# Optimization experiments

Hardware: AMD Instinct MI355X
Metric: run time of the kernel (lower is better)

The kernel has to match this reference:

```python
import jax, jax.numpy as jnp
import numpy as np

B, L, D, DIN, S, R, K = 2, 1024, 1024, 2048, 16, 64, 4


def setup_inputs() -> dict:
    key = jax.random.key(0)
    ks = jax.random.split(key, 8)
    f = lambda k, sh, sc: jax.random.normal(k, sh, jnp.float32) * sc
    return {
        "x": f(ks[0], (B, L, D), 1.0),
        "norm_w": jnp.ones((D,), jnp.float32),
        "W_in": f(ks[1], (D, 2 * DIN), D ** -0.5),
        "conv_w": f(ks[2], (DIN, 1, K), 0.5),
        "conv_b": jnp.zeros((DIN,), jnp.float32),
        "W_x": f(ks[3], (DIN, R + 2 * S), DIN ** -0.5),
        "W_dt": f(ks[4], (R, DIN), R ** -0.5),
        "b_dt": f(ks[5], (DIN,), 0.1),
        "A_log": jnp.log(jnp.broadcast_to(jnp.arange(1, S + 1, dtype=jnp.float32), (DIN, S))),
        "D_skip": jnp.ones((DIN,), jnp.float32),
        "W_out": f(ks[6], (DIN, D), DIN ** -0.5),
    }


def reference(x, norm_w, W_in, conv_w, conv_b, W_x, W_dt, b_dt, A_log, D_skip, W_out):
    eps = 1e-5
    # RMSNorm
    xn = x * jax.lax.rsqrt(jnp.mean(x * x, axis=-1, keepdims=True) + eps) * norm_w
    # input projection -> (x_branch, gate)
    xz = xn @ W_in                       # [B,L,2*DIN]
    xi, z = jnp.split(xz, 2, axis=-1)
    # causal depthwise conv1d along L
    xt = jnp.transpose(xi, (0, 2, 1))    # [B,DIN,L]
    xc = jax.lax.conv_general_dilated(xt, conv_w, (1,), [(K - 1, 0)],
                                      feature_group_count=DIN)
    xc = jnp.transpose(xc, (0, 2, 1)) + conv_b
    xc = jax.nn.silu(xc)                 # [B,L,DIN]
    # input-dependent SSM parameters
    xd = xc @ W_x                        # [B,L,R+2S]
    dt, Bm, Cm = jnp.split(xd, [R, R + S], axis=-1)
    dt = jax.nn.softplus(dt @ W_dt + b_dt)           # [B,L,DIN]
    A = -jnp.exp(A_log)                              # [DIN,S]
    dA = jnp.exp(dt[..., None] * A)                  # [B,L,DIN,S]
    dBu = (dt * xc)[..., None] * Bm[:, :, None, :]   # [B,L,DIN,S]
    # selective scan: h_t = dA_t * h_{t-1} + dBu_t (parallel associative scan)
    def comb(c1, c2):
        a1, b1 = c1
        a2, b2 = c2
        return a1 * a2, a2 * b1 + b2
    _, h = jax.lax.associative_scan(comb, (dA, dBu), axis=1)
    y = jnp.einsum('blds,bls->bld', h, Cm) + D_skip * xc
    y = y * jax.nn.silu(z)
    return x + y @ W_out
```

## Files before the change

kernel.cpp:

```cpp
#include <hip/hip_runtime.h>

#define B_    2
#define L_    1024
#define D_    1024
#define DIN_  2048
#define S_    16
#define R_    64
#define NTOK  (B_ * L_)
#define NCH   32
#define LC    (L_ / NCH)

typedef unsigned short u16;
typedef short bf16x8 __attribute__((ext_vector_type(8)));
typedef float f32x4  __attribute__((ext_vector_type(4)));

__device__ __forceinline__ u16 f2bf(float f) {
    union { float f; unsigned u; } v; v.f = f;
    return (u16)((v.u + 0x7FFFu + ((v.u >> 16) & 1u)) >> 16);
}
__device__ __forceinline__ float bf2f(u16 b) {
    union { unsigned u; float f; } v; v.u = (unsigned)b << 16;
    return v.f;
}

__global__ __launch_bounds__(256) void rmsnorm_kernel(
    const float* __restrict__ x, const float* __restrict__ w, u16* __restrict__ xn) {
    int row = blockIdx.x;
    const float4 v = ((const float4*)(x + (size_t)row * D_))[threadIdx.x];
    float ss = v.x * v.x + v.y * v.y + v.z * v.z + v.w * v.w;
#pragma unroll
    for (int o = 32; o > 0; o >>= 1) ss += __shfl_down(ss, o);
    __shared__ float red[4];
    if ((threadIdx.x & 63) == 0) red[threadIdx.x >> 6] = ss;
    __syncthreads();
    float tot = red[0] + red[1] + red[2] + red[3];
    float sc = rsqrtf(tot * (1.f / (float)D_) + 1e-5f);
    const float4 wv = ((const float4*)w)[threadIdx.x];
    ushort4 o;
    o.x = f2bf(v.x * sc * wv.x);
    o.y = f2bf(v.y * sc * wv.y);
    o.z = f2bf(v.z * sc * wv.z);
    o.w = f2bf(v.w * sc * wv.w);
    ((ushort4*)(xn + (size_t)row * D_))[threadIdx.x] = o;
}

__device__ __forceinline__ void transp_tile(
    const float* __restrict__ src, u16* __restrict__ dst,
    int R, int Csrc, int cx, int cy, int tx, int ty) {
    __shared__ float tile[32][33];
    int c0 = cx * 32, r0 = cy * 32;
#pragma unroll
    for (int i = 0; i < 32; i += 8)
        tile[ty + i][tx] = (c0 + tx < Csrc)
            ? src[(size_t)(r0 + ty + i) * Csrc + c0 + tx] : 0.f;
    __syncthreads();
#pragma unroll
    for (int i = 0; i < 32; i += 8)
        dst[(size_t)(c0 + ty + i) * R + r0 + tx] = f2bf(tile[tx][ty + i]);
}

__global__ __launch_bounds__(256) void transpose_all_kernel(
    const float* __restrict__ W_in,  u16* __restrict__ WinT,
    const float* __restrict__ W_out, u16* __restrict__ WoutT,
    const float* __restrict__ W_x,   u16* __restrict__ WxT,
    const float* __restrict__ W_dt,  u16* __restrict__ WdtT) {
    int bid = blockIdx.x;
    int tx = threadIdx.x & 31, ty = threadIdx.x >> 5;
    if (bid < 4096) {
        transp_tile(W_in, WinT, D_, 2 * DIN_, bid % 128, bid / 128, tx, ty);
    } else if (bid < 6144) {
        int b = bid - 4096;
        transp_tile(W_out, WoutT, DIN_, D_, b % 32, b / 32, tx, ty);
    } else if (bid < 6400) {
        int b = bid - 6144;
        transp_tile(W_x, WxT, DIN_, 96, b % 4, b / 4, tx, ty);
    } else {
        int b = bid - 6400;
        transp_tile(W_dt, WdtT, R_, DIN_, b % 64, b / 64, tx, ty);
    }
}

#define BK 32
template<int BM, int BN, int CX>
__global__ __launch_bounds__(256) void gemm_bf16(
    const u16* __restrict__ A, int lda,
    const u16* __restrict__ Bt, int ldb,
    float* __restrict__ C, u16* __restrict__ Cbf, int ldc,
    const float* __restrict__ aux,
    int M, int N, int K, int mode) {
    constexpr int WGM = (BM >= 128) ? 2 : 1;
    constexpr int WGN = 4 / WGM;
    constexpr int FM = BM / (16 * WGM);
    constexpr int FN = BN / (16 * WGN);
    constexpr int ABYTES = BM * BK * 2;
    constexpr int BBYTES = BN * BK * 2;
    __shared__ __align__(16) u16 As[2][BM * BK];
    __shared__ __align__(16) u16 Bs[2][BN * BK];
    const int t = threadIdx.x;
    const int w = t >> 6;
    const int l = t & 63;
    const int lr = l & 15;
    const int kg = l >> 4;
    const int wm = (w / WGN) * (BM / WGM);
    const int wn = (w % WGN) * (BN / WGN);

    const int GX = gridDim.x, GY = gridDim.y;
    int h = blockIdx.x + GX * (blockIdx.y + GY * blockIdx.z);
    int xcd = h & 7, pos = h >> 3;
    int ncx = GX / CX;
    int chunk = (GX * GY * gridDim.z) >> 3;
    int rpc = chunk / CX;
    int bx = (xcd % ncx) * CX + pos % CX;
    int r  = (xcd / ncx) * rpc + pos / CX;
    int by = r % GY;
    int bz = r / GY;

    const int row0 = by * BM;
    const int col0 = bx * BN;
    const int kbase = bz * K;

    auto stage = [&](int buf, int k0) {
#pragma unroll
        for (int i = 0; i < ABYTES; i += 4096) {
            int off = i + t * 16;
            int grow = off >> 6;
            int sw = ((off >> 4) & 3) ^ ((grow >> 1) & 3);
            const u16* ga = A + (size_t)(row0 + grow) * lda + k0 + sw * 8;
            __builtin_amdgcn_global_load_lds(
                (const __attribute__((address_space(1))) unsigned int*)(const void*)ga,
                (__attribute__((address_space(3))) unsigned int*)(void*)&As[buf][off >> 1],
                16, 0, 0);
        }
#pragma unroll
        for (int i = 0; i < BBYTES; i += 4096) {
            int off = i + t * 16;
            int grow = off >> 6;
            int sw = ((off >> 4) & 3) ^ ((grow >> 1) & 3);
            const u16* gb = Bt + (size_t)(col0 + grow) * ldb + k0 + sw * 8;
            __builtin_amdgcn_global_load_lds(
                (const __attribute__((address_space(1))) unsigned int*)(const void*)gb,
                (__attribute__((address_space(3))) unsigned int*)(void*)&Bs[buf][off >> 1],
                16, 0, 0);
        }
    };

    f32x4 acc[FM][FN];
#pragma unroll
    for (int i = 0; i < FM; ++i)
#pragma unroll
        for (int j = 0; j < FN; ++j) acc[i][j] = (f32x4){0.f, 0.f, 0.f, 0.f};

    const int nt = K / BK;
    stage(0, kbase);
    asm volatile("s_waitcnt vmcnt(0)" ::: "memory");
    __builtin_amdgcn_s_barrier();
    asm volatile("" ::: "memory");

    int cur = 0;
    for (int tt = 0; tt < nt; ++tt) {
        if (tt + 1 < nt) stage(cur ^ 1, kbase + (tt + 1) * BK);
        bf16x8 af[FM], bfr[FN];
#pragma unroll
        for (int mt = 0; mt < FM; ++mt) {
            int ar = wm + mt * 16 + lr;
            af[mt] = *(const bf16x8*)&As[cur][ar * 32 + (kg ^ ((ar >> 1) & 3)) * 8];
        }
#pragma unroll
        for (int nt2 = 0; nt2 < FN; ++nt2) {
            int br = wn + nt2 * 16 + lr;
            bfr[nt2] = *(const bf16x8*)&Bs[cur][br * 32 + (kg ^ ((br >> 1) & 3)) * 8];
        }
        __builtin_amdgcn_s_setprio(1);
#pragma unroll
        for (int mt = 0; mt < FM; ++mt)
#pragma unroll
            for (int nt2 = 0; nt2 < FN; ++nt2)
                acc[mt][nt2] = __builtin_amdgcn_mfma_f32_16x16x32_bf16(
                    af[mt], bfr[nt2], acc[mt][nt2], 0, 0, 0);
        __builtin_amdgcn_s_setprio(0);
        if (tt + 1 < nt) {
            asm volatile("s_waitcnt vmcnt(0)" ::: "memory");
            __builtin_amdgcn_s_barrier();
            asm volatile("" ::: "memory");
        }
        cur ^= 1;
    }

    size_t pbase = (mode == 3) ? (size_t)bz * M * N : 0;
#pragma unroll
    for (int mt = 0; mt < FM; ++mt) {
#pragma unroll
        for (int nt2 = 0; nt2 < FN; ++nt2) {
#pragma unroll
            for (int r2 = 0; r2 < 4; ++r2) {
                int row = row0 + wm + mt * 16 + kg * 4 + r2;
                int col = col0 + wn + nt2 * 16 + lr;
                float v = acc[mt][nt2][r2];
                if (mode == 1) { v += aux[col]; v = (v > 20.f) ? v : log1pf(__expf(v)); }
                else if (mode == 2) { v += aux[(size_t)row * ldc + col]; }
                if (C)   C[pbase + (size_t)row * ldc + col] = v;
                if (Cbf) Cbf[(size_t)row * ldc + col] = f2bf(v);
            }
        }
    }
}

__global__ __launch_bounds__(256) void reduce_wx_kernel(
    const float* __restrict__ part, float* __restrict__ xd, u16* __restrict__ xdb) {
    int i = blockIdx.x * 256 + threadIdx.x;
    float4 s = ((const float4*)part)[i];
#pragma unroll
    for (int k = 1; k < 16; ++k) {
        float4 v = ((const float4*)(part + (size_t)k * NTOK * 128))[i];
        s.x += v.x; s.y += v.y; s.z += v.z; s.w += v.w;
    }
    ((float4*)xd)[i] = s;
    ushort4 o; o.x = f2bf(s.x); o.y = f2bf(s.y); o.z = f2bf(s.z); o.w = f2bf(s.w);
    ((ushort4*)xdb)[i] = o;
}

__global__ __launch_bounds__(256) void reduce_out_kernel(
    const float* __restrict__ part, const float* __restrict__ x, float* __restrict__ out) {
    int i = blockIdx.x * 256 + threadIdx.x;
    float4 s = ((const float4*)part)[i];
#pragma unroll
    for (int k = 1; k < 4; ++k) {
        float4 v = ((const float4*)(part + (size_t)k * NTOK * D_))[i];
        s.x += v.x; s.y += v.y; s.z += v.z; s.w += v.w;
    }
    float4 xv = ((const float4*)x)[i];
    s.x += xv.x; s.y += xv.y; s.z += xv.z; s.w += xv.w;
    ((float4*)out)[i] = s;
}

__global__ __launch_bounds__(256) void conv_silu_kernel(
    const float* __restrict__ xz, const float* __restrict__ cw,
    const float* __restrict__ cb, u16* __restrict__ xcb) {
    size_t idx = (size_t)blockIdx.x * 256 + threadIdx.x;
    int c = (int)(idx & (DIN_ - 1));
    int g = (int)(idx >> 11);
    int bl0 = g * 4;
    int l0 = bl0 & (L_ - 1);
    const float4 w = ((const float4*)cw)[c];
    float bias = cb[c];
    float v[7];
#pragma unroll
    for (int k = 0; k < 7; ++k) {
        int off = k - 3;
        v[k] = (l0 + off >= 0) ? xz[(size_t)(bl0 + off) * 4096 + c] : 0.f;
    }
#pragma unroll
    for (int j = 0; j < 4; ++j) {
        float acc = bias + v[j] * w.x + v[j + 1] * w.y + v[j + 2] * w.z + v[j + 3] * w.w;
        float s = acc / (1.f + __expf(-acc));
        xcb[(size_t)(bl0 + j) * DIN_ + c] = f2bf(s);
    }
}

__global__ __launch_bounds__(256) void scan_chunk_kernel(
    const float* __restrict__ dt, const u16* __restrict__ xcb,
    const float* __restrict__ xd, const float* __restrict__ A_log,
    float* __restrict__ Pout, float* __restrict__ Hout) {
    int din = blockIdx.x * 256 + threadIdx.x;
    int c = blockIdx.y, b = blockIdx.z;
    float a[S_], h[S_];
#pragma unroll
    for (int q = 0; q < 4; ++q) {
        float4 av = ((const float4*)(A_log + (size_t)din * S_))[q];
        a[q * 4 + 0] = -__expf(av.x); a[q * 4 + 1] = -__expf(av.y);
        a[q * 4 + 2] = -__expf(av.z); a[q * 4 + 3] = -__expf(av.w);
    }
#pragma unroll
    for (int s = 0; s < S_; ++s) h[s] = 0.f;
    float sdt = 0.f;
    size_t rbase = (size_t)b * L_ + (size_t)c * LC;
#pragma unroll 2
    for (int i = 0; i < LC; ++i) {
        size_t row = rbase + i;
        float dtv = dt[row * DIN_ + din];
        float xcv = bf2f(xcb[row * DIN_ + din]);
        float du = dtv * xcv;
        sdt += dtv;
        const float4* bp = (const float4*)(xd + row * 128 + 64);
        float4 B0 = bp[0], B1 = bp[1], B2 = bp[2], B3 = bp[3];
        float Bv[S_] = {B0.x, B0.y, B0.z, B0.w, B1.x, B1.y, B1.z, B1.w,
                        B2.x, B2.y, B2.z, B2.w, B3.x, B3.y, B3.z, B3.w};
#pragma unroll
        for (int s = 0; s < S_; ++s) {
            float dA = __expf(dtv * a[s]);
            h[s] = h[s] * dA + du * Bv[s];
        }
    }
    size_t obase = ((size_t)(b * NCH + c) * DIN_ + din) * S_;
#pragma unroll
    for (int q = 0; q < 4; ++q) {
        float4 pv, hv;
        pv.x = __expf(a[q * 4 + 0] * sdt); pv.y = __expf(a[q * 4 + 1] * sdt);
        pv.z = __expf(a[q * 4 + 2] * sdt); pv.w = __expf(a[q * 4 + 3] * sdt);
        hv.x = h[q * 4 + 0]; hv.y = h[q * 4 + 1]; hv.z = h[q * 4 + 2]; hv.w = h[q * 4 + 3];
        ((float4*)(Pout + obase))[q] = pv;
        ((float4*)(Hout + obase))[q] = hv;
    }
}

__global__ __launch_bounds__(256) void scan_combine_kernel(
    const float* __restrict__ P, const float* __restrict__ H,
    float* __restrict__ h0) {
    int tid = blockIdx.x * 256 + threadIdx.x;
    int ds = tid & (DIN_ * S_ - 1);
    int b = tid >> 15;
    float h = 0.f;
#pragma unroll
    for (int c = 0; c < NCH; ++c) {
        size_t idx = ((size_t)(b * NCH + c) * DIN_ * S_) + ds;
        h0[idx] = h;
        h = H[idx] + P[idx] * h;
    }
}

__global__ __launch_bounds__(256) void scan_final_kernel(
    const float* __restrict__ dt, const u16* __restrict__ xcb,
    const float* __restrict__ xd, const float* __restrict__ A_log,
    const float* __restrict__ h0, const float* __restrict__ Dskip,
    const float* __restrict__ xz, u16* __restrict__ yg) {
    int din = blockIdx.x * 256 + threadIdx.x;
    int c = blockIdx.y, b = blockIdx.z;
    float a[S_], h[S_];
#pragma unroll
    for (int q = 0; q < 4; ++q) {
        float4 av = ((const float4*)(A_log + (size_t)din * S_))[q];
        a[q * 4 + 0] = -__expf(av.x); a[q * 4 + 1] = -__expf(av.y);
        a[q * 4 + 2] = -__expf(av.z); a[q * 4 + 3] = -__expf(av.w);
    }
    size_t ibase = ((size_t)(b * NCH + c) * DIN_ + din) * S_;
#pragma unroll
    for (int q = 0; q < 4; ++q) {
        float4 hv = ((const float4*)(h0 + ibase))[q];
        h[q * 4 + 0] = hv.x; h[q * 4 + 1] = hv.y; h[q * 4 + 2] = hv.z; h[q * 4 + 3] = hv.w;
    }
    float dsk = Dskip[din];
    size_t rbase = (size_t)b * L_ + (size_t)c * LC;
#pragma unroll 2
    for (int i = 0; i < LC; ++i) {
        size_t row = rbase + i;
        float dtv = dt[row * DIN_ + din];
        float xcv = bf2f(xcb[row * DIN_ + din]);
        float du = dtv * xcv;
        const float4* bp = (const float4*)(xd + row * 128 + 64);
        float4 B0 = bp[0], B1 = bp[1], B2 = bp[2], B3 = bp[3];
        const float4* cp = (const float4*)(xd + row * 128 + 80);
        float4 C0 = cp[0], C1 = cp[1], C2 = cp[2], C3 = cp[3];
        float Bv[S_] = {B0.x, B0.y, B0.z, B0.w, B1.x, B1.y, B1.z, B1.w,
                        B2.x, B2.y, B2.z, B2.w, B3.x, B3.y, B3.z, B3.w};
        float Cv[S_] = {C0.x, C0.y, C0.z, C0.w, C1.x, C1.y, C1.z, C1.w,
                        C2.x, C2.y, C2.z, C2.w, C3.x, C3.y, C3.z, C3.w};
        float py = 0.f;
#pragma unroll
        for (int s = 0; s < S_; ++s) {
            float dA = __expf(dtv * a[s]);
            h[s] = h[s] * dA + du * Bv[s];
            py += h[s] * Cv[s];
        }
        float zv = xz[row * 4096 + DIN_ + din];
        float y = (py + dsk * xcv) * (zv / (1.f + __expf(-zv)));
        yg[row * DIN_ + din] = f2bf(y);
    }
}

extern "C" void kernel_launch(void* const* d_in, const int* in_sizes, int n_in,
                              void* d_out, int out_size, void* d_ws, size_t ws_size,
                              hipStream_t stream) {
    const float* x      = (const float*)d_in[0];
    const float* norm_w = (const float*)d_in[1];
    const float* W_in   = (const float*)d_in[2];
    const float* conv_w = (const float*)d_in[3];
    const float* conv_b = (const float*)d_in[4];
    const float* W_x    = (const float*)d_in[5];
    const float* W_dt   = (const float*)d_in[6];
    const float* b_dt   = (const float*)d_in[7];
    const float* A_log  = (const float*)d_in[8];
    const float* D_skip = (const float*)d_in[9];
    const float* W_out  = (const float*)d_in[10];
    float* out = (float*)d_out;

    char* p = (char*)d_ws;
    auto alloc = [&](size_t bytes) {
        char* r = p;
        p += (bytes + 255) & ~(size_t)255;
        return r;
    };
    u16*   xn    = (u16*)alloc((size_t)NTOK * D_ * 2);
    u16*   WinT  = (u16*)alloc((size_t)2 * DIN_ * D_ * 2);
    u16*   WoutT = (u16*)alloc((size_t)D_ * DIN_ * 2);
    u16*   WxT   = (u16*)alloc((size_t)128 * DIN_ * 2);
    u16*   WdtT  = (u16*)alloc((size_t)DIN_ * R_ * 2);
    float* xz    = (float*)alloc((size_t)NTOK * 2 * DIN_ * 4);
    u16*   xcb   = (u16*)alloc((size_t)NTOK * DIN_ * 2);
    float* xd    = (float*)alloc((size_t)NTOK * 128 * 4);
    u16*   xdb   = (u16*)alloc((size_t)NTOK * 128 * 2);
    float* dtb   = (float*)alloc((size_t)NTOK * DIN_ * 4);
    u16*   yg    = (u16*)alloc((size_t)NTOK * DIN_ * 2);
    float* Pbuf  = (float*)alloc((size_t)B_ * NCH * DIN_ * S_ * 4);
    float* Hbuf  = (float*)alloc((size_t)B_ * NCH * DIN_ * S_ * 4);
    float* h0buf = (float*)alloc((size_t)B_ * NCH * DIN_ * S_ * 4);

    float* part_wx  = dtb;
    float* part_out = xz;

    rmsnorm_kernel<<<NTOK, 256, 0, stream>>>(x, norm_w, xn);
    transpose_all_kernel<<<6528, 256, 0, stream>>>(
        W_in, WinT, W_out, WoutT, W_x, WxT, W_dt, WdtT);

    gemm_bf16<64, 128, 8><<<dim3(2 * DIN_ / 128, NTOK / 64), 256, 0, stream>>>(
        xn, D_, WinT, D_, xz, nullptr, 2 * DIN_, nullptr, NTOK, 2 * DIN_, D_, 0);
    conv_silu_kernel<<<(NTOK * DIN_ / 4) / 256, 256, 0, stream>>>(xz, conv_w, conv_b, xcb);
    gemm_bf16<64, 128, 1><<<dim3(1, NTOK / 64, 16), 256, 0, stream>>>(
        xcb, DIN_, WxT, DIN_, part_wx, nullptr, 128, nullptr, NTOK, 128, DIN_ / 16, 3);
    reduce_wx_kernel<<<(NTOK * 128 / 4) / 256, 256, 0, stream>>>(part_wx, xd, xdb);
    gemm_bf16<64, 128, 8><<<dim3(DIN_ / 128, NTOK / 64), 256, 0, stream>>>(
        xdb, 128, WdtT, R_, dtb, nullptr, DIN_, b_dt, NTOK, DIN_, R_, 1);
    {
        dim3 grid(DIN_ / 256, NCH, B_);
        scan_chunk_kernel<<<grid, 256, 0, stream>>>(dtb, xcb, xd, A_log, Pbuf, Hbuf);
        scan_combine_kernel<<<(B_ * DIN_ * S_) / 256, 256, 0, stream>>>(Pbuf, Hbuf, h0buf);
        scan_final_kernel<<<grid, 256, 0, stream>>>(dtb, xcb, xd, A_log, h0buf, D_skip, xz, yg);
    }
    gemm_bf16<64, 128, 8><<<dim3(D_ / 128, NTOK / 64, 4), 256, 0, stream>>>(
        yg, DIN_, WoutT, DIN_, part_out, nullptr, D_, nullptr, NTOK, D_, DIN_ / 4, 3);
    reduce_out_kernel<<<(NTOK * D_ / 4) / 256, 256, 0, stream>>>(part_out, x, out);
}
```

Measured before the change: 178.7 us.

## Store xz and dt intermediates as bf16 and merge rmsnorm into prep kernel

The input-projection GEMM now writes its output xz in bf16, and the dt projection GEMM writes dt in bf16. The conv, chunked-scan and final-scan kernels read these bf16 buffers instead of fp32, which cuts their memory traffic in half. RMSNorm is folded into the weight-transpose kernel as extra blocks, removing one launch, and the partial-sum buffers get their own allocation. The cost is lower precision for dt and the gate/x branch, and the change relies on the GEMM's bf16 output path (Cbf) handling modes 0 and 1.

```diff
diff --git a/kernel.cpp b/kernel.cpp
--- a/kernel.cpp
+++ b/kernel.cpp
@@ -23,27 +23,6 @@
     return v.f;
 }
 
-__global__ __launch_bounds__(256) void rmsnorm_kernel(
-    const float* __restrict__ x, const float* __restrict__ w, u16* __restrict__ xn) {
-    int row = blockIdx.x;
-    const float4 v = ((const float4*)(x + (size_t)row * D_))[threadIdx.x];
-    float ss = v.x * v.x + v.y * v.y + v.z * v.z + v.w * v.w;
-#pragma unroll
-    for (int o = 32; o > 0; o >>= 1) ss += __shfl_down(ss, o);
-    __shared__ float red[4];
-    if ((threadIdx.x & 63) == 0) red[threadIdx.x >> 6] = ss;
-    __syncthreads();
-    float tot = red[0] + red[1] + red[2] + red[3];
-    float sc = rsqrtf(tot * (1.f / (float)D_) + 1e-5f);
-    const float4 wv = ((const float4*)w)[threadIdx.x];
-    ushort4 o;
-    o.x = f2bf(v.x * sc * wv.x);
-    o.y = f2bf(v.y * sc * wv.y);
-    o.z = f2bf(v.z * sc * wv.z);
-    o.w = f2bf(v.w * sc * wv.w);
-    ((ushort4*)(xn + (size_t)row * D_))[threadIdx.x] = o;
-}
-
 __device__ __forceinline__ void transp_tile(
     const float* __restrict__ src, u16* __restrict__ dst,
     int R, int Csrc, int cx, int cy, int tx, int ty) {
@@ -59,23 +38,45 @@
         dst[(size_t)(c0 + ty + i) * R + r0 + tx] = f2bf(tile[tx][ty + i]);
 }
 
-__global__ __launch_bounds__(256) void transpose_all_kernel(
+__global__ __launch_bounds__(256) void prep_kernel(
+    const float* __restrict__ x, const float* __restrict__ nw, u16* __restrict__ xn,
     const float* __restrict__ W_in,  u16* __restrict__ WinT,
     const float* __restrict__ W_out, u16* __restrict__ WoutT,
     const float* __restrict__ W_x,   u16* __restrict__ WxT,
     const float* __restrict__ W_dt,  u16* __restrict__ WdtT) {
     int bid = blockIdx.x;
+    if (bid < NTOK) {
+        int row = bid;
+        const float4 v = ((const float4*)(x + (size_t)row * D_))[threadIdx.x];
+        float ss = v.x * v.x + v.y * v.y + v.z * v.z + v.w * v.w;
+#pragma unroll
+        for (int o = 32; o > 0; o >>= 1) ss += __shfl_down(ss, o);
+        __shared__ float red[4];
+        if ((threadIdx.x & 63) == 0) red[threadIdx.x >> 6] = ss;
+        __syncthreads();
+        float tot = red[0] + red[1] + red[2] + red[3];
+        float sc = rsqrtf(tot * (1.f / (float)D_) + 1e-5f);
+        const float4 wv = ((const float4*)nw)[threadIdx.x];
+        ushort4 o;
+        o.x = f2bf(v.x * sc * wv.x);
+        o.y = f2bf(v.y * sc * wv.y);
+        o.z = f2bf(v.z * sc * wv.z);
+        o.w = f2bf(v.w * sc * wv.w);
+        ((ushort4*)(xn + (size_t)row * D_))[threadIdx.x] = o;
+        return;
+    }
+    int b2 = bid - NTOK;
     int tx = threadIdx.x & 31, ty = threadIdx.x >> 5;
-    if (bid < 4096) {
-        transp_tile(W_in, WinT, D_, 2 * DIN_, bid % 128, bid / 128, tx, ty);
-    } else if (bid < 6144) {
-        int b = bid - 4096;
+    if (b2 < 4096) {
+        transp_tile(W_in, WinT, D_, 2 * DIN_, b2 % 128, b2 / 128, tx, ty);
+    } else if (b2 < 6144) {
+        int b = b2 - 4096;
         transp_tile(W_out, WoutT, DIN_, D_, b % 32, b / 32, tx, ty);
-    } else if (bid < 6400) {
-        int b = bid - 6144;
+    } else if (b2 < 6400) {
+        int b = b2 - 6144;
         transp_tile(W_x, WxT, DIN_, 96, b % 4, b / 4, tx, ty);
     } else {
-        int b = bid - 6400;
+        int b = b2 - 6400;
         transp_tile(W_dt, WdtT, R_, DIN_, b % 64, b / 64, tx, ty);
     }
 }
@@ -234,7 +235,7 @@
 }
 
 __global__ __launch_bounds__(256) void conv_silu_kernel(
-    const float* __restrict__ xz, const float* __restrict__ cw,
+    const u16* __restrict__ xzb, const float* __restrict__ cw,
     const float* __restrict__ cb, u16* __restrict__ xcb) {
     size_t idx = (size_t)blockIdx.x * 256 + threadIdx.x;
     int c = (int)(idx & (DIN_ - 1));
@@ -247,7 +248,7 @@
 #pragma unroll
     for (int k = 0; k < 7; ++k) {
         int off = k - 3;
-        v[k] = (l0 + off >= 0) ? xz[(size_t)(bl0 + off) * 4096 + c] : 0.f;
+        v[k] = (l0 + off >= 0) ? bf2f(xzb[(size_t)(bl0 + off) * 4096 + c]) : 0.f;
     }
 #pragma unroll
     for (int j = 0; j < 4; ++j) {
@@ -258,7 +259,7 @@
 }
 
 __global__ __launch_bounds__(256) void scan_chunk_kernel(
-    const float* __restrict__ dt, const u16* __restrict__ xcb,
+    const u16* __restrict__ dtq, const u16* __restrict__ xcb,
     const float* __restrict__ xd, const float* __restrict__ A_log,
     float* __restrict__ Pout, float* __restrict__ Hout) {
     int din = blockIdx.x * 256 + threadIdx.x;
@@ -277,7 +278,7 @@
 #pragma unroll 2
     for (int i = 0; i < LC; ++i) {
         size_t row = rbase + i;
-        float dtv = dt[row * DIN_ + din];
+        float dtv = bf2f(dtq[row * DIN_ + din]);
         float xcv = bf2f(xcb[row * DIN_ + din]);
         float du = dtv * xcv;
         sdt += dtv;
@@ -319,10 +320,10 @@
 }
 
 __global__ __launch_bounds__(256) void scan_final_kernel(
-    const float* __restrict__ dt, const u16* __restrict__ xcb,
+    const u16* __restrict__ dtq, const u16* __restrict__ xcb,
     const float* __restrict__ xd, const float* __restrict__ A_log,
     const float* __restrict__ h0, const float* __restrict__ Dskip,
-    const float* __restrict__ xz, u16* __restrict__ yg) {
+    const u16* __restrict__ xzb, u16* __restrict__ yg) {
     int din = blockIdx.x * 256 + threadIdx.x;
     int c = blockIdx.y, b = blockIdx.z;
     float a[S_], h[S_];
@@ -343,7 +344,7 @@
 #pragma unroll 2
     for (int i = 0; i < LC; ++i) {
         size_t row = rbase + i;
-        float dtv = dt[row * DIN_ + din];
+        float dtv = bf2f(dtq[row * DIN_ + din]);
         float xcv = bf2f(xcb[row * DIN_ + din]);
         float du = dtv * xcv;
         const float4* bp = (const float4*)(xd + row * 128 + 64);
@@ -361,7 +362,7 @@
             h[s] = h[s] * dA + du * Bv[s];
             py += h[s] * Cv[s];
         }
-        float zv = xz[row * 4096 + DIN_ + din];
+        float zv = bf2f(xzb[row * 4096 + DIN_ + din]);
         float y = (py + dsk * xcv) * (zv / (1.f + __expf(-zv)));
         yg[row * DIN_ + din] = f2bf(y);
     }
@@ -389,41 +390,39 @@
         p += (bytes + 255) & ~(size_t)255;
         return r;
     };
-    u16*   xn    = (u16*)alloc((size_t)NTOK * D_ * 2);
-    u16*   WinT  = (u16*)alloc((size_t)2 * DIN_ * D_ * 2);
-    u16*   WoutT = (u16*)alloc((size_t)D_ * DIN_ * 2);
-    u16*   WxT   = (u16*)alloc((size_t)128 * DIN_ * 2);
-    u16*   WdtT  = (u16*)alloc((size_t)DIN_ * R_ * 2);
-    float* xz    = (float*)alloc((size_t)NTOK * 2 * DIN_ * 4);
-    u16*   xcb   = (u16*)alloc((size_t)NTOK * DIN_ * 2);
-    float* xd    = (float*)alloc((size_t)NTOK * 128 * 4);
-    u16*   xdb   = (u16*)alloc((size_t)NTOK * 128 * 2);
-    float* dtb   = (float*)alloc((size_t)NTOK * DIN_ * 4);
-    u16*   yg    = (u16*)alloc((size_t)NTOK * DIN_ * 2);
-    float* Pbuf  = (float*)alloc((size_t)B_ * NCH * DIN_ * S_ * 4);
-    float* Hbuf  = (float*)alloc((size_t)B_ * NCH * DIN_ * S_ * 4);
-    float* h0buf = (float*)alloc((size_t)B_ * NCH * DIN_ * S_ * 4);
-
-    float* part_wx  = dtb;
-    float* part_out = xz;
-
-    rmsnorm_kernel<<<NTOK, 256, 0, stream>>>(x, norm_w, xn);
-    transpose_all_kernel<<<6528, 256, 0, stream>>>(
-        W_in, WinT, W_out, WoutT, W_x, WxT, W_dt, WdtT);
+    u16*   xn      = (u16*)alloc((size_t)NTOK * D_ * 2);
+    u16*   WinT    = (u16*)alloc((size_t)2 * DIN_ * D_ * 2);
+    u16*   WoutT   = (u16*)alloc((size_t)D_ * DIN_ * 2);
+    u16*   WxT     = (u16*)alloc((size_t)128 * DIN_ * 2);
+    u16*   WdtT    = (u16*)alloc((size_t)DIN_ * R_ * 2);
+    u16*   xzb     = (u16*)alloc((size_t)NTOK * 2 * DIN_ * 2);
+    u16*   xcb     = (u16*)alloc((size_t)NTOK * DIN_ * 2);
+    float* xd      = (float*)alloc((size_t)NTOK * 128 * 4);
+    u16*   xdb     = (u16*)alloc((size_t)NTOK * 128 * 2);
+    u16*   dtq     = (u16*)alloc((size_t)NTOK * DIN_ * 2);
+    u16*   yg      = (u16*)alloc((size_t)NTOK * DIN_ * 2);
+    float* Pbuf    = (float*)alloc((size_t)B_ * NCH * DIN_ * S_ * 4);
+    float* Hbuf    = (float*)alloc((size_t)B_ * NCH * DIN_ * S_ * 4);
+    float* h0buf   = (float*)alloc((size_t)B_ * NCH * DIN_ * S_ * 4);
+    float* part_out = (float*)alloc((size_t)4 * NTOK * D_ * 4);
+    float* part_wx  = part_out;
+
+    prep_kernel<<<NTOK + 6528, 256, 0, stream>>>(
+        x, norm_w, xn, W_in, WinT, W_out, WoutT, W_x, WxT, W_dt, WdtT);
 
     gemm_bf16<64, 128, 8><<<dim3(2 * DIN_ / 128, NTOK / 64), 256, 0, stream>>>(
-        xn, D_, WinT, D_, xz, nullptr, 2 * DIN_, nullptr, NTOK, 2 * DIN_, D_, 0);
-    conv_silu_kernel<<<(NTOK * DIN_ / 4) / 256, 256, 0, stream>>>(xz, conv_w, conv_b, xcb);
+        xn, D_, WinT, D_, nullptr, xzb, 2 * DIN_, nullptr, NTOK, 2 * DIN_, D_, 0);
+    conv_silu_kernel<<<(NTOK * DIN_ / 4) / 256, 256, 0, stream>>>(xzb, conv_w, conv_b, xcb);
     gemm_bf16<64, 128, 1><<<dim3(1, NTOK / 64, 16), 256, 0, stream>>>(
         xcb, DIN_, WxT, DIN_, part_wx, nullptr, 128, nullptr, NTOK, 128, DIN_ / 16, 3);
     reduce_wx_kernel<<<(NTOK * 128 / 4) / 256, 256, 0, stream>>>(part_wx, xd, xdb);
     gemm_bf16<64, 128, 8><<<dim3(DIN_ / 128, NTOK / 64), 256, 0, stream>>>(
-        xdb, 128, WdtT, R_, dtb, nullptr, DIN_, b_dt, NTOK, DIN_, R_, 1);
+        xdb, 128, WdtT, R_, nullptr, dtq, DIN_, b_dt, NTOK, DIN_, R_, 1);
     {
         dim3 grid(DIN_ / 256, NCH, B_);
-        scan_chunk_kernel<<<grid, 256, 0, stream>>>(dtb, xcb, xd, A_log, Pbuf, Hbuf);
+        scan_chunk_kernel<<<grid, 256, 0, stream>>>(dtq, xcb, xd, A_log, Pbuf, Hbuf);
         scan_combine_kernel<<<(B_ * DIN_ * S_) / 256, 256, 0, stream>>>(Pbuf, Hbuf, h0buf);
-        scan_final_kernel<<<grid, 256, 0, stream>>>(dtb, xcb, xd, A_log, h0buf, D_skip, xz, yg);
+        scan_final_kernel<<<grid, 256, 0, stream>>>(dtq, xcb, xd, A_log, h0buf, D_skip, xzb, yg);
     }
     gemm_bf16<64, 128, 8><<<dim3(D_ / 128, NTOK / 64, 4), 256, 0, stream>>>(
         yg, DIN_, WoutT, DIN_, part_out, nullptr, D_, nullptr, NTOK, D_, DIN_ / 4, 3);
```

Result: faster. 170.7 us (-4.4%).
